# Kernel optimization log

Hardware: AMD Instinct MI355X
Metric: run time of the kernel (lower is better)

The kernel has to match this reference:

```python
import jax, jax.numpy as jnp
import numpy as np

ALPHA = 0.5
DIM = -1
TOL = 1e-4
MAX_ITER = 5000


def stable_log_w(y, alpha):
    """Halley's method root of h(x) = -alpha*x + (y-alpha) - (1-alpha)*exp(x)."""

    def resid(x):
        return -alpha * x + (y - alpha) - (1.0 - alpha) * jnp.exp(x)

    x0 = jnp.minimum(y / alpha - 1.0, y - 1.0)

    def cond(st):
        x, it = st
        # torch breaks when max|f| <= tol -> continue while > tol
        return (jnp.max(jnp.abs(resid(x))) > TOL) & (it < MAX_ITER)

    def body(st):
        x, it = st
        e = jnp.exp(x)
        f = -alpha * x + (y - alpha) - (1.0 - alpha) * e
        df = -alpha - (1.0 - alpha) * e
        ddf = -(1.0 - alpha) * e
        x = x - 2.0 * f * df / (2.0 * df * df - f * ddf)
        return (x, it + 1)

    x, _ = jax.lax.while_loop(cond, body, (x0, jnp.int32(0)))
    return x


def prox_softmax_core(y, alpha, dim):
    """Newton over nu s.t. sum_i exp(g(y_i + nu)) = 1. Returns (p, nu, l)."""

    def eval_at(nu):
        l = stable_log_w(y + nu, alpha)
        p = jnp.exp(l)
        f = jnp.sum(p, axis=dim, keepdims=True) - 1.0
        return l, p, f

    nu0 = 1.0 - jnp.max(y, axis=dim, keepdims=True)
    l0, p0, f0 = eval_at(nu0)

    def cond(st):
        nu, l, p, f, it = st
        # torch breaks when max|f| < tol -> continue while >= tol
        return (jnp.max(jnp.abs(f)) >= TOL) & (it < MAX_ITER)

    def body(st):
        nu, l, p, f, it = st
        df = jnp.sum(p / (y + nu - alpha * l), axis=dim, keepdims=True)
        nu = nu - f / df
        l, p, f = eval_at(nu)
        return (nu, l, p, f, it + 1)

    nu, l, p, f, _ = jax.lax.while_loop(cond, body, (nu0, l0, p0, f0, jnp.int32(0)))
    return p, nu, l


def setup_inputs() -> dict:
    key = jax.random.key(0)
    x = jax.random.normal(key, (8192, 4096), dtype=jnp.float32)
    return {"x": x}


def reference(x):
    p, _, _ = prox_softmax_core(x, ALPHA, DIM)
    return p
```

## Files before the change

kernel.cpp:

```cpp
#include <hip/hip_runtime.h>
#include <math.h>

#define TPB 256
#define EPT 16
#define COLS 4096
#define NWAVE (TPB / 64)

typedef float vfloat4 __attribute__((ext_vector_type(4)));

__device__ __forceinline__ float wave_sum(float v) {
#pragma unroll
    for (int o = 32; o > 0; o >>= 1) v += __shfl_xor(v, o, 64);
    return v;
}
__device__ __forceinline__ float wave_max(float v) {
#pragma unroll
    for (int o = 32; o > 0; o >>= 1) v = fmaxf(v, __shfl_xor(v, o, 64));
    return v;
}
__device__ __forceinline__ void block_red2(float& a, float& b, float* sred, int wid, int lane) {
    a = wave_sum(a); b = wave_sum(b);
    if (lane == 0) { sred[wid] = a; sred[NWAVE + wid] = b; }
    __syncthreads();
    a = (sred[0] + sred[1]) + (sred[2] + sred[3]);
    b = (sred[4] + sred[5]) + (sred[6] + sred[7]);
    __syncthreads();
}
__device__ __forceinline__ void block_red_summax(float& a, float& b, float* sred, int wid, int lane) {
    a = wave_sum(a); b = wave_max(b);
    if (lane == 0) { sred[wid] = a; sred[NWAVE + wid] = b; }
    __syncthreads();
    a = (sred[0] + sred[1]) + (sred[2] + sred[3]);
    b = fmaxf(fmaxf(sred[4], sred[5]), fmaxf(sred[6], sred[7]));
    __syncthreads();
}

__device__ __forceinline__ float halley_hw(float p, float t) {
    float e = __expf(p);
    float w = p * e;
    float f = w - t;
    float fp = w + e;
    float den = fmaf(fp, fp, -0.5f * f * (fp + e));
    return p - __fdividef(f * fp, den);
}

__global__ __launch_bounds__(TPB) void prox_softmax_kernel(
    const float* __restrict__ X, float* __restrict__ P, int rows)
{
    __shared__ float sred[2 * NWAVE];
    const int tid = threadIdx.x;
    const int row = blockIdx.x;
    if (row >= rows) return;
    const int wid = tid >> 6, lane = tid & 63;

    const float4* __restrict__ x4 = reinterpret_cast<const float4*>(X + (size_t)row * COLS);
    vfloat4* __restrict__ p4 = reinterpret_cast<vfloat4*>(P + (size_t)row * COLS);

    float q[EPT], p[EPT];

#pragma unroll
    for (int j = 0; j < 4; ++j) {
        float4 v = x4[tid + j * TPB];
        q[4 * j + 0] = v.x; q[4 * j + 1] = v.y;
        q[4 * j + 2] = v.z; q[4 * j + 3] = v.w;
    }

    const float C2E = 2.8853900817779268f;
    float A = 0.f, B = 0.f, C = 0.f, qm = 0.f;
#pragma unroll
    for (int j = 0; j < EPT; ++j) {
        float e = __builtin_amdgcn_exp2f(q[j] * C2E);
        q[j] = e;
        float e2 = e * e;
        A += e;
        B += e2;
        C = fmaf(e2, e, C);
        qm = fmaxf(qm, e);
    }
    block_red2(A, B, sred, wid, lane);
    block_red_summax(C, qm, sred, wid, lane);

    float disc = fmaf(A, A, -4.f * B);
    float s0 = __fdividef(2.f, A + sqrtf(fmaxf(disc, 0.f)));
    float s = s0;
#pragma unroll
    for (int k = 0; k < 3; ++k) {
        float g  = fmaf(fmaf(fmaf(1.5f * C, s, -B), s, A), s, -1.f);
        float gp = fmaf(fmaf(4.5f * C, s, -2.f * B), s, A);
        s -= __fdividef(g, gp);
    }
    if (!(s > 0.f && s < 3.4e38f)) s = s0;
    s = fminf(fmaxf(s, 0.25f * s0), 4.f * s0);

    float S1 = 0.f, S2 = 0.f;
#pragma unroll
    for (int j = 0; j < EPT; ++j) {
        float t = q[j] * s;
        float acc = fmaf(23.343054f, t, -10.8f);
        acc = fmaf(acc, t, 125.f / 24.f);
        acc = fmaf(acc, t, -8.f / 3.f);
        acc = fmaf(acc, t, 1.5f);
        acc = fmaf(acc, t, -1.f);
        acc = fmaf(acc, t, 1.f);
        float pp = t * acc;
        p[j] = pp;
        float rr = pp * fmaf(pp, pp - 1.f, 1.f);
        S1 += pp;
        S2 += rr;
    }
    block_red2(S1, S2, sred, wid, lane);
    float f = S1 - 1.f;
    float tmax = qm * s;

    if ((tmax < 0.22f) && (fabsf(f) < 5e-3f)) {
        float dsig = -__fdividef(f, S2);
#pragma unroll
        for (int j = 0; j < EPT; ++j) {
            float pp = p[j];
            float rr = pp * fmaf(pp, pp - 1.f, 1.f);
            p[j] = fmaf(rr, dsig, pp);
        }
    } else {
#pragma unroll
        for (int j = 0; j < EPT; ++j)
            p[j] = __logf(1.f + q[j] * s);
        for (int it = 0; it < 10; ++it) {
            S1 = 0.f; S2 = 0.f;
#pragma unroll
            for (int j = 0; j < EPT; ++j) {
                float t = q[j] * s;
                float pp = halley_hw(p[j], t);
                pp = halley_hw(pp, t);
                p[j] = pp;
                S1 += pp;
                S2 += __fdividef(pp, 1.f + pp);
            }
            block_red2(S1, S2, sred, wid, lane);
            f = S1 - 1.f;
            if (fabsf(f) < 2e-5f) break;
            float dsig = fminf(fmaxf(-__fdividef(f, S2), -1.f), 1.f);
            s *= __expf(dsig);
        }
    }

#pragma unroll
    for (int j = 0; j < 4; ++j) {
        vfloat4 v;
        v.x = p[4 * j + 0]; v.y = p[4 * j + 1];
        v.z = p[4 * j + 2]; v.w = p[4 * j + 3];
        __builtin_nontemporal_store(v, &p4[tid + j * TPB]);
    }
}

extern "C" void kernel_launch(void* const* d_in, const int* in_sizes, int n_in,
                              void* d_out, int out_size, void* d_ws, size_t ws_size,
                              hipStream_t stream) {
    const float* x = (const float*)d_in[0];
    float* out = (float*)d_out;
    int rows = out_size / COLS;
    prox_softmax_kernel<<<rows, TPB, 0, stream>>>(x, out, rows);
}
```

Baseline: 49.91 us.

## Map one row per wavefront and drop block-level reductions

Each row is now handled by a single 64-lane wavefront holding 64 elements per lane, so all reductions become wave shuffles with no shared memory or __syncthreads. The cubic Newton refinement of the initial scale is dropped, and the cheap correction path is taken for much larger residuals (0.05 instead of 5e-3). In the fallback Halley path, t is recomputed from reloaded input instead of being kept in registers, which lowers register pressure. The trade-offs are much higher per-thread register use (64-element arrays), lower occupancy, and looser accuracy from the relaxed correction threshold.

```diff
diff --git a/kernel.cpp b/kernel.cpp
--- a/kernel.cpp
+++ b/kernel.cpp
@@ -2,9 +2,9 @@
 #include <math.h>
 
 #define TPB 256
-#define EPT 16
+#define WPB (TPB / 64)
+#define EPL 64
 #define COLS 4096
-#define NWAVE (TPB / 64)
 
 typedef float vfloat4 __attribute__((ext_vector_type(4)));
 
@@ -17,22 +17,6 @@
 #pragma unroll
     for (int o = 32; o > 0; o >>= 1) v = fmaxf(v, __shfl_xor(v, o, 64));
     return v;
-}
-__device__ __forceinline__ void block_red2(float& a, float& b, float* sred, int wid, int lane) {
-    a = wave_sum(a); b = wave_sum(b);
-    if (lane == 0) { sred[wid] = a; sred[NWAVE + wid] = b; }
-    __syncthreads();
-    a = (sred[0] + sred[1]) + (sred[2] + sred[3]);
-    b = (sred[4] + sred[5]) + (sred[6] + sred[7]);
-    __syncthreads();
-}
-__device__ __forceinline__ void block_red_summax(float& a, float& b, float* sred, int wid, int lane) {
-    a = wave_sum(a); b = wave_max(b);
-    if (lane == 0) { sred[wid] = a; sred[NWAVE + wid] = b; }
-    __syncthreads();
-    a = (sred[0] + sred[1]) + (sred[2] + sred[3]);
-    b = fmaxf(fmaxf(sred[4], sred[5]), fmaxf(sred[6], sred[7]));
-    __syncthreads();
 }
 
 __device__ __forceinline__ float halley_hw(float p, float t) {
@@ -47,54 +31,40 @@
 __global__ __launch_bounds__(TPB) void prox_softmax_kernel(
     const float* __restrict__ X, float* __restrict__ P, int rows)
 {
-    __shared__ float sred[2 * NWAVE];
-    const int tid = threadIdx.x;
-    const int row = blockIdx.x;
+    const int lane = threadIdx.x & 63;
+    const int row = blockIdx.x * WPB + (threadIdx.x >> 6);
     if (row >= rows) return;
-    const int wid = tid >> 6, lane = tid & 63;
 
     const float4* __restrict__ x4 = reinterpret_cast<const float4*>(X + (size_t)row * COLS);
     vfloat4* __restrict__ p4 = reinterpret_cast<vfloat4*>(P + (size_t)row * COLS);
 
-    float q[EPT], p[EPT];
+    float q[EPL];
 
 #pragma unroll
-    for (int j = 0; j < 4; ++j) {
-        float4 v = x4[tid + j * TPB];
+    for (int j = 0; j < 16; ++j) {
+        float4 v = x4[lane + j * 64];
         q[4 * j + 0] = v.x; q[4 * j + 1] = v.y;
         q[4 * j + 2] = v.z; q[4 * j + 3] = v.w;
     }
 
     const float C2E = 2.8853900817779268f;
-    float A = 0.f, B = 0.f, C = 0.f, qm = 0.f;
+    float A = 0.f, B = 0.f, qm = 0.f;
 #pragma unroll
-    for (int j = 0; j < EPT; ++j) {
+    for (int j = 0; j < EPL; ++j) {
         float e = __builtin_amdgcn_exp2f(q[j] * C2E);
         q[j] = e;
-        float e2 = e * e;
         A += e;
-        B += e2;
-        C = fmaf(e2, e, C);
+        B = fmaf(e, e, B);
         qm = fmaxf(qm, e);
     }
-    block_red2(A, B, sred, wid, lane);
-    block_red_summax(C, qm, sred, wid, lane);
+    A = wave_sum(A); B = wave_sum(B); qm = wave_max(qm);
 
     float disc = fmaf(A, A, -4.f * B);
-    float s0 = __fdividef(2.f, A + sqrtf(fmaxf(disc, 0.f)));
-    float s = s0;
-#pragma unroll
-    for (int k = 0; k < 3; ++k) {
-        float g  = fmaf(fmaf(fmaf(1.5f * C, s, -B), s, A), s, -1.f);
-        float gp = fmaf(fmaf(4.5f * C, s, -2.f * B), s, A);
-        s -= __fdividef(g, gp);
-    }
-    if (!(s > 0.f && s < 3.4e38f)) s = s0;
-    s = fminf(fmaxf(s, 0.25f * s0), 4.f * s0);
+    float s = __fdividef(2.f, A + sqrtf(fmaxf(disc, 0.f)));
 
     float S1 = 0.f, S2 = 0.f;
 #pragma unroll
-    for (int j = 0; j < EPT; ++j) {
+    for (int j = 0; j < EPL; ++j) {
         float t = q[j] * s;
         float acc = fmaf(23.343054f, t, -10.8f);
         acc = fmaf(acc, t, 125.f / 24.f);
@@ -103,39 +73,52 @@
         acc = fmaf(acc, t, -1.f);
         acc = fmaf(acc, t, 1.f);
         float pp = t * acc;
-        p[j] = pp;
-        float rr = pp * fmaf(pp, pp - 1.f, 1.f);
+        q[j] = pp;
         S1 += pp;
-        S2 += rr;
+        S2 += pp * fmaf(pp, pp - 1.f, 1.f);
     }
-    block_red2(S1, S2, sred, wid, lane);
+    S1 = wave_sum(S1); S2 = wave_sum(S2);
     float f = S1 - 1.f;
     float tmax = qm * s;
 
-    if ((tmax < 0.22f) && (fabsf(f) < 5e-3f)) {
+    if ((tmax < 0.22f) && (fabsf(f) < 0.05f)) {
         float dsig = -__fdividef(f, S2);
 #pragma unroll
-        for (int j = 0; j < EPT; ++j) {
-            float pp = p[j];
+        for (int j = 0; j < EPL; ++j) {
+            float pp = q[j];
             float rr = pp * fmaf(pp, pp - 1.f, 1.f);
-            p[j] = fmaf(rr, dsig, pp);
+            q[j] = fmaf(rr, dsig, pp);
         }
     } else {
+        float ls = __log2f(s);
 #pragma unroll
-        for (int j = 0; j < EPT; ++j)
-            p[j] = __logf(1.f + q[j] * s);
+        for (int j = 0; j < 16; ++j) {
+            float4 v = x4[lane + j * 64];
+#pragma unroll
+            for (int k = 0; k < 4; ++k) {
+                float xv = (k == 0) ? v.x : (k == 1) ? v.y : (k == 2) ? v.z : v.w;
+                float t = __builtin_amdgcn_exp2f(fmaf(xv, C2E, ls));
+                q[4 * j + k] = __logf(1.f + t);
+            }
+        }
         for (int it = 0; it < 10; ++it) {
             S1 = 0.f; S2 = 0.f;
+            float ls2 = __log2f(s);
 #pragma unroll
-            for (int j = 0; j < EPT; ++j) {
-                float t = q[j] * s;
-                float pp = halley_hw(p[j], t);
-                pp = halley_hw(pp, t);
-                p[j] = pp;
-                S1 += pp;
-                S2 += __fdividef(pp, 1.f + pp);
+            for (int j = 0; j < 16; ++j) {
+                float4 v = x4[lane + j * 64];
+#pragma unroll
+                for (int k = 0; k < 4; ++k) {
+                    float xv = (k == 0) ? v.x : (k == 1) ? v.y : (k == 2) ? v.z : v.w;
+                    float t = __builtin_amdgcn_exp2f(fmaf(xv, C2E, ls2));
+                    float pp = halley_hw(q[4 * j + k], t);
+                    pp = halley_hw(pp, t);
+                    q[4 * j + k] = pp;
+                    S1 += pp;
+                    S2 += __fdividef(pp, 1.f + pp);
+                }
             }
-            block_red2(S1, S2, sred, wid, lane);
+            S1 = wave_sum(S1); S2 = wave_sum(S2);
             f = S1 - 1.f;
             if (fabsf(f) < 2e-5f) break;
             float dsig = fminf(fmaxf(-__fdividef(f, S2), -1.f), 1.f);
@@ -144,11 +127,11 @@
     }
 
 #pragma unroll
-    for (int j = 0; j < 4; ++j) {
+    for (int j = 0; j < 16; ++j) {
         vfloat4 v;
-        v.x = p[4 * j + 0]; v.y = p[4 * j + 1];
-        v.z = p[4 * j + 2]; v.w = p[4 * j + 3];
-        __builtin_nontemporal_store(v, &p4[tid + j * TPB]);
+        v.x = q[4 * j + 0]; v.y = q[4 * j + 1];
+        v.z = q[4 * j + 2]; v.w = q[4 * j + 3];
+        __builtin_nontemporal_store(v, &p4[lane + j * 64]);
     }
 }
 
@@ -158,5 +141,6 @@
     const float* x = (const float*)d_in[0];
     float* out = (float*)d_out;
     int rows = out_size / COLS;
-    prox_softmax_kernel<<<rows, TPB, 0, stream>>>(x, out, rows);
+    int blocks = (rows + WPB - 1) / WPB;
+    prox_softmax_kernel<<<blocks, TPB, 0, stream>>>(x, out, rows);
 }
```

New measurement: 79.42 us. 59.1% more time.
